# Kernel optimization log

Measured on AMD Instinct MI355X. Metric: run time of the kernel, lower is better.

The kernel has to match this reference:

```python
import jax, jax.numpy as jnp
import numpy as np

N = 50000        # nodes
E = 800000       # edges (before self-loops)
IN = 128         # in_dim
HID = 32         # hidden_dim per head
HEADS = 4
OUT = 64         # out_dim
NEG_SLOPE = 0.2  # PyG GATConv default leaky_relu slope


def setup_inputs() -> dict:
    key = jax.random.key(0)
    ks = jax.random.split(key, 10)
    g = lambda k, shape: jax.random.normal(k, shape, jnp.float32) * 0.1
    x = jax.random.normal(ks[0], (N, IN), jnp.float32)
    edge_index = jax.random.randint(ks[1], (2, E), 0, N, dtype=jnp.int64)
    W1 = g(ks[2], (IN, HEADS * HID))
    att_src1 = g(ks[3], (HEADS, HID))
    att_dst1 = g(ks[4], (HEADS, HID))
    b1 = jnp.zeros((HEADS * HID,), jnp.float32)
    W2 = g(ks[5], (HEADS * HID, OUT))
    att_src2 = g(ks[6], (1, OUT))
    att_dst2 = g(ks[7], (1, OUT))
    b2 = jnp.zeros((OUT,), jnp.float32)
    return {"x": x, "edge_index": edge_index,
            "W1": W1, "att_src1": att_src1, "att_dst1": att_dst1, "b1": b1,
            "W2": W2, "att_src2": att_src2, "att_dst2": att_dst2, "b2": b2}


def gat_layer(x, src, dst, W, a_src, a_dst, b, concat):
    """One PyG-style GATConv layer (self-loops already in src/dst)."""
    H, C = a_src.shape
    h = (x @ W).reshape(-1, H, C)                       # [N, H, C]
    al_s = jnp.sum(h * a_src, axis=-1)                  # [N, H]
    al_d = jnp.sum(h * a_dst, axis=-1)                  # [N, H]
    e = jax.nn.leaky_relu(al_s[src] + al_d[dst], NEG_SLOPE)  # [E', H]
    # segment softmax over incoming edges of each destination node
    m = jax.ops.segment_max(e, dst, num_segments=N)
    m = jnp.where(jnp.isfinite(m), m, 0.0)
    ex = jnp.exp(e - m[dst])
    denom = jax.ops.segment_sum(ex, dst, num_segments=N)
    alpha = ex / (denom[dst] + 1e-16)                   # [E', H]
    out = jax.ops.segment_sum(alpha[:, :, None] * h[src], dst, num_segments=N)  # [N,H,C]
    out = out.reshape(-1, H * C) if concat else out.mean(axis=1)
    return out + b


def reference(x, edge_index, W1, att_src1, att_dst1, b1, W2, att_src2, att_dst2, b2):
    src, dst = edge_index[0], edge_index[1]
    loop = jnp.arange(N, dtype=src.dtype)               # add_self_loops=True default
    src = jnp.concatenate([src, loop])
    dst = jnp.concatenate([dst, loop])
    h = gat_layer(x, src, dst, W1, att_src1, att_dst1, b1, concat=True)   # [N, HEADS*HID]
    h = jax.nn.elu(h)
    return gat_layer(h, src, dst, W2, att_src2, att_dst2, b2, concat=False)  # [N, OUT]
```

## Files before the change

kernel.cpp:

```cpp
#include <hip/hip_runtime.h>

#define NN 50000
#define EE 800000
#define NB 196
#define CHUNK 2048
#define NBLK ((EE + CHUNK - 1) / CHUNK)
#define GB1 ((NN + 63) / 64)
#define CAP 6144
#define CAPB 40
#define SSTR 6400

typedef unsigned int uint;
typedef unsigned short ushort;
typedef __attribute__((ext_vector_type(8))) short bf16x8;
typedef __attribute__((ext_vector_type(4))) float f32x4;

__device__ __forceinline__ float lrelu(float v){ return v > 0.f ? v : 0.2f*v; }
__device__ __forceinline__ ushort bf16r(float a){
  uint ua = __float_as_uint(a);
  return (ushort)((ua + 0x7FFFu + ((ua >> 16) & 1u)) >> 16);
}
__device__ __forceinline__ uint pack_bf16(float a, float b){
  return (uint)bf16r(a) | ((uint)bf16r(b) << 16);
}
__device__ __forceinline__ float bf_lo(uint u){ return __uint_as_float(u << 16); }
__device__ __forceinline__ float bf_hi(uint u){ return __uint_as_float(u & 0xFFFF0000u); }

union BG1Shared {
  struct { int h[NB]; int sc[256]; int gdelta[NB]; uint P[CHUNK]; int A[CHUNK]; } bk;
  struct { ushort Wt[128*136]; ushort Ash[64*136]; } gm;
};

__global__ __launch_bounds__(256, 3) void k_bg1(const int* __restrict__ ei,
    int* __restrict__ cnt, uint* __restrict__ ebuf,
    const float* __restrict__ x, const float* __restrict__ W,
    const float* __restrict__ a_src, const float* __restrict__ a_dst,
    uint* __restrict__ h1b, float* __restrict__ al_s, float* __restrict__ al_d,
    const float* __restrict__ W2, uint* __restrict__ w2b){
  __shared__ BG1Shared S;
  int t = threadIdx.x;
  if (blockIdx.x == NBLK + GB1){
    for (int idx = t; idx < 4096; idx += 256){
      int n = idx >> 6, kp = idx & 63;
      float a = W2[(2*kp)*64 + n];
      float b = W2[(2*kp+1)*64 + n];
      w2b[n*64 + kp] = pack_bf16(a, b);
    }
    return;
  }
  if (blockIdx.x < NBLK){
    if (t < NB) S.bk.h[t] = 0;
    __syncthreads();
    int base = blockIdx.x * CHUNK;
    int end = base + CHUNK; if (end > EE) end = EE;
    int bc = end - base;
    int be[8]; int re[8]; uint pe[8];
    #pragma unroll
    for (int q = 0; q < 8; ++q){
      int i = base + t + q*256;
      be[q] = -1;
      if (i < end){
        int s_ = ei[i], d_ = ei[EE + i];
        pe[q] = ((uint)d_ << 16) | (uint)s_;
        int bb = d_ >> 8;
        be[q] = bb;
        re[q] = atomicAdd(&S.bk.h[bb], 1);
      }
    }
    __syncthreads();
    int v = (t < NB) ? S.bk.h[t] : 0;
    S.bk.sc[t] = v;
    __syncthreads();
    for (int off = 1; off < 256; off <<= 1){
      int add = (t >= off) ? S.bk.sc[t-off] : 0;
      __syncthreads();
      S.bk.sc[t] += add;
      __syncthreads();
    }
    if (t < NB){
      int lofs = S.bk.sc[t] - v;
      S.bk.gdelta[t] = (t*NBLK + blockIdx.x)*CAPB - lofs;
      S.bk.h[t] = lofs;
      cnt[blockIdx.x*NB + t] = v;
    }
    __syncthreads();
    #pragma unroll
    for (int q = 0; q < 8; ++q) if (be[q] >= 0){
      int j = S.bk.h[be[q]] + re[q];
      S.bk.P[j] = pe[q];
      S.bk.A[j] = S.bk.gdelta[be[q]] + j;
    }
    __syncthreads();
    for (int j = t; j < bc; j += 256) ebuf[S.bk.A[j]] = S.bk.P[j];
    return;
  }
  int row0 = (blockIdx.x - NBLK) * 64;
  const float4* W4 = (const float4*)W;
  #pragma unroll
  for (int f0 = 0; f0 < 4096; f0 += 256){
    int idx4 = f0 + t;
    int k = idx4 >> 5;
    int n0 = (idx4 & 31) * 4;
    float4 v = W4[idx4];
    S.gm.Wt[(n0  )*136 + k] = bf16r(v.x);
    S.gm.Wt[(n0+1)*136 + k] = bf16r(v.y);
    S.gm.Wt[(n0+2)*136 + k] = bf16r(v.z);
    S.gm.Wt[(n0+3)*136 + k] = bf16r(v.w);
  }
  const float4* x4 = (const float4*)x;
  #pragma unroll
  for (int f0 = 0; f0 < 2048; f0 += 256){
    int idx4 = f0 + t;
    int row = idx4 >> 5;
    int q = idx4 & 31;
    float4 v = make_float4(0.f,0.f,0.f,0.f);
    if (row0 + row < NN) v = x4[(size_t)(row0+row)*32 + q];
    *(uint2*)(S.gm.Ash + row*136 + q*4) = make_uint2(pack_bf16(v.x, v.y), pack_bf16(v.z, v.w));
  }
  __syncthreads();

  int w = t >> 6, lane = t & 63;
  int lm = lane & 15, lg = lane >> 4;
  const ushort* Ab = S.gm.Ash + (w*16 + lm)*136 + lg*8;
  const ushort* Bb = S.gm.Wt + lm*136 + lg*8;
  f32x4 acc[8];
  #pragma unroll
  for (int i = 0; i < 8; ++i) acc[i] = (f32x4){0.f,0.f,0.f,0.f};
  #pragma unroll
  for (int ks = 0; ks < 4; ++ks){
    bf16x8 af = *(const bf16x8*)(Ab + ks*32);
    #pragma unroll
    for (int ct = 0; ct < 8; ++ct){
      bf16x8 bfr = *(const bf16x8*)(Bb + ct*16*136 + ks*32);
      acc[ct] = __builtin_amdgcn_mfma_f32_16x16x32_bf16(af, bfr, acc[ct], 0, 0, 0);
    }
  }
  int nbase = row0 + w*16 + lg*4;
  float ps[4][4], pd[4][4];
  #pragma unroll
  for (int h = 0; h < 4; ++h)
    #pragma unroll
    for (int r = 0; r < 4; ++r){ ps[h][r] = 0.f; pd[h][r] = 0.f; }
  #pragma unroll
  for (int ct = 0; ct < 8; ++ct){
    int col = ct*16 + lm;
    float ac = a_src[col], dc = a_dst[col];
    #pragma unroll
    for (int r = 0; r < 4; ++r){
      float v = acc[ct][r];
      ps[ct>>1][r] += v*ac;
      pd[ct>>1][r] += v*dc;
      float vp = __shfl_xor(v, 1);
      if ((lm & 1) == 0 && nbase + r < NN)
        h1b[(size_t)(nbase+r)*64 + ct*8 + (lm>>1)] = pack_bf16(v, vp);
    }
  }
  #pragma unroll
  for (int h = 0; h < 4; ++h)
    #pragma unroll
    for (int r = 0; r < 4; ++r){
      float s = ps[h][r], d = pd[h][r];
      s += __shfl_xor(s,1); s += __shfl_xor(s,2); s += __shfl_xor(s,4); s += __shfl_xor(s,8);
      d += __shfl_xor(d,1); d += __shfl_xor(d,2); d += __shfl_xor(d,4); d += __shfl_xor(d,8);
      if (lm == 0 && nbase + r < NN){
        al_s[(nbase+r)*4 + h] = s;
        al_d[(nbase+r)*4 + h] = d;
      }
    }
}

__global__ __launch_bounds__(256) void k_csr(const int* __restrict__ cnt,
                                             const uint* __restrict__ ebuf,
                                             int* __restrict__ rptr, int* __restrict__ rend,
                                             ushort* __restrict__ csr){
  __shared__ uint  sbuf[CAP];
  __shared__ ushort rnk[CAP];
  __shared__ int h[256];
  __shared__ int sc[256];
  __shared__ int btot;
  int b = blockIdx.x, t = threadIdx.x;
  int nd0 = b * 256;
  int ncnt = NN - nd0; if (ncnt > 256) ncnt = 256;
  int c0 = (t < NBLK) ? cnt[t*NB + b] : 0;
  int c1 = (t + 256 < NBLK) ? cnt[(t+256)*NB + b] : 0;
  if (c0 > CAPB) c0 = CAPB;
  if (c1 > CAPB) c1 = CAPB;
  int mysum = c0 + c1;
  sc[t] = mysum;
  __syncthreads();
  for (int off = 1; off < 256; off <<= 1){
    int add = (t >= off) ? sc[t-off] : 0;
    __syncthreads();
    sc[t] += add;
    __syncthreads();
  }
  int base = sc[t] - mysum;
  if (t == 255) btot = sc[255];
  __syncthreads();
  int tot = btot; if (tot > CAP) tot = CAP;
  for (int j = 0; j < c0; ++j)
    if (base + j < CAP) sbuf[base + j] = ebuf[(size_t)(b*NBLK + t)*CAPB + j];
  for (int j = 0; j < c1; ++j)
    if (base + c0 + j < CAP) sbuf[base + c0 + j] = ebuf[(size_t)(b*NBLK + t + 256)*CAPB + j];
  h[t] = (t < ncnt) ? 1 : 0;
  __syncthreads();
  for (int j = t; j < tot; j += 256){
    int local = (sbuf[j] >> 16) & 255;
    rnk[j] = (ushort)atomicAdd(&h[local], 1);
  }
  __syncthreads();
  int v = h[t];
  sc[t] = v;
  __syncthreads();
  for (int off = 1; off < 256; off <<= 1){
    int add = (t >= off) ? sc[t-off] : 0;
    __syncthreads();
    sc[t] += add;
    __syncthreads();
  }
  h[t] = sc[t] - v;
  __syncthreads();
  int cb = b * SSTR;
  if (t < ncnt){
    int rs = cb + h[t];
    rptr[nd0 + t] = rs;
    rend[nd0 + t] = rs + v;
    csr[rs] = (ushort)(nd0 + t);
  }
  for (int j = t; j < tot; j += 256){
    uint p = sbuf[j];
    int local = (p >> 16) & 255;
    csr[cb + h[local] + (int)rnk[j]] = (ushort)(p & 0xFFFFu);
  }
}

__global__ __launch_bounds__(512, 2) void k_ag12(const int* __restrict__ rptr, const int* __restrict__ rend,
    const ushort* __restrict__ csr,
    const uint* __restrict__ h1b, const float* __restrict__ al1s, const float* __restrict__ al1d,
    const float* __restrict__ b1, const uint* __restrict__ w2b,
    const float* __restrict__ a2s, const float* __restrict__ a2d,
    uint* __restrict__ gb, float* __restrict__ al2s, float* __restrict__ al2d){
  __shared__ ushort Wt[64*136];
  __shared__ ushort Ash[64*136];
  __shared__ float ssum[64], dsum[64];
  int tid = threadIdx.x;
  int nd0 = blockIdx.x * 64;
  if (tid < 64){ ssum[tid] = 0.f; dsum[tid] = 0.f; }
  const uint4* Wg = (const uint4*)w2b;
  #pragma unroll
  for (int f0 = 0; f0 < 1024; f0 += 512){
    int f = f0 + tid;
    int row = f >> 4, q = f & 15;
    uint4 v = Wg[f];
    *(uint4*)(Wt + row*136 + q*8) = v;
  }
  int w = tid >> 6, lane = tid & 63;
  int half = lane >> 5;
  int li   = lane & 31;
  int h    = li >> 3;
  uint rowoff = (uint)(li*2);
  uint* AshU = (uint*)Ash;
  for (int i = 0; i < 8; ++i){
    int nloc = w*8 + i;
    int wid = nd0 + nloc;
    if (wid >= NN) break;
    float ad = al1d[(uint)(wid*4 + h)];
    int rs = rptr[wid];
    int deg = rend[wid] - rs;
    float a0 = 0.f, a1 = 0.f, a2 = 0.f, a3 = 0.f, den = 0.f;
    for (int b0 = 0; b0 < deg; b0 += 64){
      int nb = deg - b0; if (nb > 64) nb = 64;
      int sv = (lane < nb) ? (int)csr[(uint)(rs + b0 + lane)] : 0;
      int jj = 0;
      for (; jj + 8 <= nb; jj += 8){
        int j = jj + half;
        int s0 = __shfl(sv, j), s1 = __shfl(sv, j+2), s2 = __shfl(sv, j+4), s3 = __shfl(sv, j+6);
        float e0 = al1s[(uint)(s0*4 + h)];
        float e1 = al1s[(uint)(s1*4 + h)];
        float e2 = al1s[(uint)(s2*4 + h)];
        float e3 = al1s[(uint)(s3*4 + h)];
        uint2 u0 = *(const uint2*)(h1b + (((uint)s0) << 6) + rowoff);
        uint2 u1 = *(const uint2*)(h1b + (((uint)s1) << 6) + rowoff);
        uint2 u2 = *(const uint2*)(h1b + (((uint)s2) << 6) + rowoff);
        uint2 u3 = *(const uint2*)(h1b + (((uint)s3) << 6) + rowoff);
        float x0 = __expf(lrelu(e0 + ad));
        float x1 = __expf(lrelu(e1 + ad));
        float x2 = __expf(lrelu(e2 + ad));
        float x3 = __expf(lrelu(e3 + ad));
        den += x0 + x1 + x2 + x3;
        a0 += x0*bf_lo(u0.x) + x1*bf_lo(u1.x) + x2*bf_lo(u2.x) + x3*bf_lo(u3.x);
        a1 += x0*bf_hi(u0.x) + x1*bf_hi(u1.x) + x2*bf_hi(u2.x) + x3*bf_hi(u3.x);
        a2 += x0*bf_lo(u0.y) + x1*bf_lo(u1.y) + x2*bf_lo(u2.y) + x3*bf_lo(u3.y);
        a3 += x0*bf_hi(u0.y) + x1*bf_hi(u1.y) + x2*bf_hi(u2.y) + x3*bf_hi(u3.y);
      }
      for (; jj < nb; jj += 2){
        int j = jj + half;
        bool ok = j < nb;
        int s0 = __shfl(sv, ok ? j : 0);
        float e = al1s[(uint)(s0*4 + h)];
        uint2 u = *(const uint2*)(h1b + (((uint)s0) << 6) + rowoff);
        float ex = ok ? __expf(lrelu(e + ad)) : 0.f;
        den += ex;
        a0 += ex*bf_lo(u.x); a1 += ex*bf_hi(u.x);
        a2 += ex*bf_lo(u.y); a3 += ex*bf_hi(u.y);
      }
    }
    den += __shfl_xor(den, 32);
    a0  += __shfl_xor(a0, 32);
    a1  += __shfl_xor(a1, 32);
    a2  += __shfl_xor(a2, 32);
    a3  += __shfl_xor(a3, 32);
    if (half == 0){
      float inv = 1.f/(den + 1e-16f);
      float4 bb = *(const float4*)(b1 + li*4);
      float o0 = a0*inv + bb.x, o1 = a1*inv + bb.y, o2 = a2*inv + bb.z, o3 = a3*inv + bb.w;
      o0 = o0 > 0.f ? o0 : (__expf(o0) - 1.f);
      o1 = o1 > 0.f ? o1 : (__expf(o1) - 1.f);
      o2 = o2 > 0.f ? o2 : (__expf(o2) - 1.f);
      o3 = o3 > 0.f ? o3 : (__expf(o3) - 1.f);
      *(uint2*)(AshU + nloc*68 + li*2) = make_uint2(pack_bf16(o0,o1), pack_bf16(o2,o3));
    }
  }
  __syncthreads();
  int lm = lane & 15, lg = lane >> 4;
  int rw = w & 3, cw = w >> 2;
  const ushort* Ab = Ash + (rw*16 + lm)*136 + lg*8;
  const ushort* Bb = Wt + (cw*32 + lm)*136 + lg*8;
  f32x4 acc[2];
  acc[0] = (f32x4){0.f,0.f,0.f,0.f};
  acc[1] = (f32x4){0.f,0.f,0.f,0.f};
  #pragma unroll
  for (int ks = 0; ks < 4; ++ks){
    bf16x8 af = *(const bf16x8*)(Ab + ks*32);
    #pragma unroll
    for (int ct = 0; ct < 2; ++ct){
      bf16x8 bfr = *(const bf16x8*)(Bb + ct*16*136 + ks*32);
      acc[ct] = __builtin_amdgcn_mfma_f32_16x16x32_bf16(af, bfr, acc[ct], 0, 0, 0);
    }
  }
  int nbase = nd0 + rw*16 + lg*4;
  float ps[4], pd[4];
  #pragma unroll
  for (int r = 0; r < 4; ++r){ ps[r] = 0.f; pd[r] = 0.f; }
  #pragma unroll
  for (int ct = 0; ct < 2; ++ct){
    int col = cw*32 + ct*16 + lm;
    float ac = a2s[col], dc = a2d[col];
    #pragma unroll
    for (int r = 0; r < 4; ++r){
      float v = acc[ct][r];
      ps[r] += v*ac;
      pd[r] += v*dc;
      float vp = __shfl_xor(v, 1);
      if ((lm & 1) == 0 && nbase + r < NN)
        gb[(size_t)(nbase+r)*32 + cw*16 + ct*8 + (lm>>1)] = pack_bf16(v, vp);
    }
  }
  #pragma unroll
  for (int r = 0; r < 4; ++r){
    float s = ps[r], d = pd[r];
    s += __shfl_xor(s,1); s += __shfl_xor(s,2); s += __shfl_xor(s,4); s += __shfl_xor(s,8);
    d += __shfl_xor(d,1); d += __shfl_xor(d,2); d += __shfl_xor(d,4); d += __shfl_xor(d,8);
    if (lm == 0){
      int nloc = rw*16 + lg*4 + r;
      atomicAdd(&ssum[nloc], s);
      atomicAdd(&dsum[nloc], d);
    }
  }
  __syncthreads();
  if (tid < 64 && nd0 + tid < NN){
    al2s[nd0 + tid] = ssum[tid];
    al2d[nd0 + tid] = dsum[tid];
  }
}

__global__ __launch_bounds__(256) void k_agg2(const int* __restrict__ rptr, const int* __restrict__ rend,
    const ushort* __restrict__ csr,
    const uint* __restrict__ gb, const float* __restrict__ al_s, const float* __restrict__ al_d,
    const float* __restrict__ b2, float* __restrict__ out){
  int wid  = (blockIdx.x*256 + threadIdx.x) >> 6;
  int lane = threadIdx.x & 63;
  if (wid >= NN) return;
  int half = lane >> 5;
  int li   = lane & 31;
  float ad = al_d[(uint)wid];
  int rs = rptr[wid];
  int deg = rend[wid] - rs;
  float a0 = 0.f, a1 = 0.f, den = 0.f;
  for (int b0 = 0; b0 < deg; b0 += 64){
    int nb = deg - b0; if (nb > 64) nb = 64;
    int sv = (lane < nb) ? (int)csr[(uint)(rs + b0 + lane)] : 0;
    int jj = 0;
    for (; jj + 8 <= nb; jj += 8){
      int j = jj + half;
      int s0 = __shfl(sv, j), s1 = __shfl(sv, j+2), s2 = __shfl(sv, j+4), s3 = __shfl(sv, j+6);
      float e0 = al_s[(uint)s0];
      float e1 = al_s[(uint)s1];
      float e2 = al_s[(uint)s2];
      float e3 = al_s[(uint)s3];
      uint u0 = gb[(((uint)s0) << 5) + (uint)li];
      uint u1 = gb[(((uint)s1) << 5) + (uint)li];
      uint u2 = gb[(((uint)s2) << 5) + (uint)li];
      uint u3 = gb[(((uint)s3) << 5) + (uint)li];
      float x0 = __expf(lrelu(e0 + ad));
      float x1 = __expf(lrelu(e1 + ad));
      float x2 = __expf(lrelu(e2 + ad));
      float x3 = __expf(lrelu(e3 + ad));
      den += x0 + x1 + x2 + x3;
      a0 += x0*bf_lo(u0) + x1*bf_lo(u1) + x2*bf_lo(u2) + x3*bf_lo(u3);
      a1 += x0*bf_hi(u0) + x1*bf_hi(u1) + x2*bf_hi(u2) + x3*bf_hi(u3);
    }
    for (; jj < nb; jj += 2){
      int j = jj + half;
      bool ok = j < nb;
      int s0 = __shfl(sv, ok ? j : 0);
      float e = al_s[(uint)s0];
      uint u = gb[(((uint)s0) << 5) + (uint)li];
      float ex = ok ? __expf(lrelu(e + ad)) : 0.f;
      den += ex;
      a0 += ex*bf_lo(u); a1 += ex*bf_hi(u);
    }
  }
  den += __shfl_xor(den, 32);
  a0  += __shfl_xor(a0, 32);
  a1  += __shfl_xor(a1, 32);
  if (half == 0){
    float inv = 1.f/(den + 1e-16f);
    float2 bb = *(const float2*)(b2 + li*2);
    *(float2*)(out + (size_t)wid*64 + li*2) = make_float2(a0*inv + bb.x, a1*inv + bb.y);
  }
}

extern "C" void kernel_launch(void* const* d_in, const int* in_sizes, int n_in,
                              void* d_out, int out_size, void* d_ws, size_t ws_size,
                              hipStream_t stream){
  const float* x   = (const float*)d_in[0];
  const int*   ei  = (const int*)d_in[1];
  const float* W1  = (const float*)d_in[2];
  const float* as1 = (const float*)d_in[3];
  const float* ad1 = (const float*)d_in[4];
  const float* b1  = (const float*)d_in[5];
  const float* W2  = (const float*)d_in[6];
  const float* as2 = (const float*)d_in[7];
  const float* ad2 = (const float*)d_in[8];
  const float* b2  = (const float*)d_in[9];
  float* out = (float*)d_out;
  (void)in_sizes; (void)n_in; (void)out_size; (void)ws_size;

  char* p = (char*)d_ws;
  size_t off = 0;
  auto alloc = [&](size_t bytes)->char*{
    char* r = p + off; off += (bytes + 255) & ~size_t(255); return r;
  };
  uint*  h1b   = (uint*)alloc((size_t)NN*64*4);
  uint*  gb    = (uint*)alloc((size_t)NN*32*4);
  uint*  w2b   = (uint*)alloc((size_t)64*64*4);
  float* al1s  = (float*)alloc((size_t)NN*4*4);
  float* al1d  = (float*)alloc((size_t)NN*4*4);
  float* al2s  = (float*)alloc((size_t)NN*4);
  float* al2d  = (float*)alloc((size_t)NN*4);
  int*   rptr  = (int*)alloc((size_t)NN*4);
  int*   rend  = (int*)alloc((size_t)NN*4);
  ushort* csr  = (ushort*)alloc((size_t)NB*SSTR*2);
  uint*  ebuf  = (uint*)alloc((size_t)NB*NBLK*CAPB*4);
  int*   cnt   = (int*)alloc((size_t)NBLK*NB*4);

  k_bg1<<<NBLK + GB1 + 1, 256, 0, stream>>>(ei, cnt, ebuf, x, W1, as1, ad1, h1b, al1s, al1d, W2, w2b);
  k_csr<<<NB, 256, 0, stream>>>(cnt, ebuf, rptr, rend, csr);
  k_ag12<<<GB1, 512, 0, stream>>>(rptr, rend, csr, h1b, al1s, al1d, b1, w2b, as2, ad2, gb, al2s, al2d);
  k_agg2<<<(NN*64+255)/256, 256, 0, stream>>>(rptr, rend, csr, gb, al2s, al2d, b2, out);
}
```

Baseline: 124.6 us.

## Load GEMM A-fragments directly from global and predicate aggregation tail loops

The layer-1 GEMM now reads each lane's x row slice straight from global memory into registers and converts it to bf16, instead of staging a 64-row x tile through shared memory. This shrinks the shared union enough to raise the occupancy hint from 3 to 4 blocks per CU. Both aggregation kernels replace the 8-wide main loop plus 2-wide remainder loop with one predicated 8-wide loop that masks out-of-range edges. The changes trade uncoalesced-ish direct global loads and some wasted masked gathers for less LDS traffic, fewer syncs and fewer tail iterations.

```diff
diff --git a/kernel.cpp b/kernel.cpp
--- a/kernel.cpp
+++ b/kernel.cpp
@@ -28,10 +28,10 @@
 
 union BG1Shared {
   struct { int h[NB]; int sc[256]; int gdelta[NB]; uint P[CHUNK]; int A[CHUNK]; } bk;
-  struct { ushort Wt[128*136]; ushort Ash[64*136]; } gm;
+  struct { ushort Wt[128*136]; } gm;
 };
 
-__global__ __launch_bounds__(256, 3) void k_bg1(const int* __restrict__ ei,
+__global__ __launch_bounds__(256, 4) void k_bg1(const int* __restrict__ ei,
     int* __restrict__ cnt, uint* __restrict__ ebuf,
     const float* __restrict__ x, const float* __restrict__ W,
     const float* __restrict__ a_src, const float* __restrict__ a_dst,
@@ -107,28 +107,25 @@
     S.gm.Wt[(n0+2)*136 + k] = bf16r(v.z);
     S.gm.Wt[(n0+3)*136 + k] = bf16r(v.w);
   }
-  const float4* x4 = (const float4*)x;
-  #pragma unroll
-  for (int f0 = 0; f0 < 2048; f0 += 256){
-    int idx4 = f0 + t;
-    int row = idx4 >> 5;
-    int q = idx4 & 31;
-    float4 v = make_float4(0.f,0.f,0.f,0.f);
-    if (row0 + row < NN) v = x4[(size_t)(row0+row)*32 + q];
-    *(uint2*)(S.gm.Ash + row*136 + q*4) = make_uint2(pack_bf16(v.x, v.y), pack_bf16(v.z, v.w));
-  }
   __syncthreads();
 
   int w = t >> 6, lane = t & 63;
   int lm = lane & 15, lg = lane >> 4;
-  const ushort* Ab = S.gm.Ash + (w*16 + lm)*136 + lg*8;
+  int myrow = row0 + w*16 + lm;
+  bool rok = myrow < NN;
+  const float* xrow = x + (size_t)(rok ? myrow : 0)*128 + lg*8;
   const ushort* Bb = S.gm.Wt + lm*136 + lg*8;
   f32x4 acc[8];
   #pragma unroll
   for (int i = 0; i < 8; ++i) acc[i] = (f32x4){0.f,0.f,0.f,0.f};
   #pragma unroll
   for (int ks = 0; ks < 4; ++ks){
-    bf16x8 af = *(const bf16x8*)(Ab + ks*32);
+    float4 f0 = rok ? *(const float4*)(xrow + ks*32)     : make_float4(0.f,0.f,0.f,0.f);
+    float4 f1 = rok ? *(const float4*)(xrow + ks*32 + 4) : make_float4(0.f,0.f,0.f,0.f);
+    union { uint4 u; bf16x8 v; } cvt;
+    cvt.u = make_uint4(pack_bf16(f0.x,f0.y), pack_bf16(f0.z,f0.w),
+                       pack_bf16(f1.x,f1.y), pack_bf16(f1.z,f1.w));
+    bf16x8 af = cvt.v;
     #pragma unroll
     for (int ct = 0; ct < 8; ++ct){
       bf16x8 bfr = *(const bf16x8*)(Bb + ct*16*136 + ks*32);
@@ -271,10 +268,11 @@
     for (int b0 = 0; b0 < deg; b0 += 64){
       int nb = deg - b0; if (nb > 64) nb = 64;
       int sv = (lane < nb) ? (int)csr[(uint)(rs + b0 + lane)] : 0;
-      int jj = 0;
-      for (; jj + 8 <= nb; jj += 8){
-        int j = jj + half;
-        int s0 = __shfl(sv, j), s1 = __shfl(sv, j+2), s2 = __shfl(sv, j+4), s3 = __shfl(sv, j+6);
+      for (int jj = 0; jj < nb; jj += 8){
+        int j0 = jj + half, j1 = j0 + 2, j2 = j0 + 4, j3 = j0 + 6;
+        bool k0 = j0 < nb, k1 = j1 < nb, k2 = j2 < nb, k3 = j3 < nb;
+        int s0 = __shfl(sv, k0 ? j0 : 0), s1 = __shfl(sv, k1 ? j1 : 0);
+        int s2 = __shfl(sv, k2 ? j2 : 0), s3 = __shfl(sv, k3 ? j3 : 0);
         float e0 = al1s[(uint)(s0*4 + h)];
         float e1 = al1s[(uint)(s1*4 + h)];
         float e2 = al1s[(uint)(s2*4 + h)];
@@ -283,26 +281,15 @@
         uint2 u1 = *(const uint2*)(h1b + (((uint)s1) << 6) + rowoff);
         uint2 u2 = *(const uint2*)(h1b + (((uint)s2) << 6) + rowoff);
         uint2 u3 = *(const uint2*)(h1b + (((uint)s3) << 6) + rowoff);
-        float x0 = __expf(lrelu(e0 + ad));
-        float x1 = __expf(lrelu(e1 + ad));
-        float x2 = __expf(lrelu(e2 + ad));
-        float x3 = __expf(lrelu(e3 + ad));
+        float x0 = k0 ? __expf(lrelu(e0 + ad)) : 0.f;
+        float x1 = k1 ? __expf(lrelu(e1 + ad)) : 0.f;
+        float x2 = k2 ? __expf(lrelu(e2 + ad)) : 0.f;
+        float x3 = k3 ? __expf(lrelu(e3 + ad)) : 0.f;
         den += x0 + x1 + x2 + x3;
         a0 += x0*bf_lo(u0.x) + x1*bf_lo(u1.x) + x2*bf_lo(u2.x) + x3*bf_lo(u3.x);
         a1 += x0*bf_hi(u0.x) + x1*bf_hi(u1.x) + x2*bf_hi(u2.x) + x3*bf_hi(u3.x);
         a2 += x0*bf_lo(u0.y) + x1*bf_lo(u1.y) + x2*bf_lo(u2.y) + x3*bf_lo(u3.y);
         a3 += x0*bf_hi(u0.y) + x1*bf_hi(u1.y) + x2*bf_hi(u2.y) + x3*bf_hi(u3.y);
-      }
-      for (; jj < nb; jj += 2){
-        int j = jj + half;
-        bool ok = j < nb;
-        int s0 = __shfl(sv, ok ? j : 0);
-        float e = al1s[(uint)(s0*4 + h)];
-        uint2 u = *(const uint2*)(h1b + (((uint)s0) << 6) + rowoff);
-        float ex = ok ? __expf(lrelu(e + ad)) : 0.f;
-        den += ex;
-        a0 += ex*bf_lo(u.x); a1 += ex*bf_hi(u.x);
-        a2 += ex*bf_lo(u.y); a3 += ex*bf_hi(u.y);
       }
     }
     den += __shfl_xor(den, 32);
@@ -390,10 +377,11 @@
   for (int b0 = 0; b0 < deg; b0 += 64){
     int nb = deg - b0; if (nb > 64) nb = 64;
     int sv = (lane < nb) ? (int)csr[(uint)(rs + b0 + lane)] : 0;
-    int jj = 0;
-    for (; jj + 8 <= nb; jj += 8){
-      int j = jj + half;
-      int s0 = __shfl(sv, j), s1 = __shfl(sv, j+2), s2 = __shfl(sv, j+4), s3 = __shfl(sv, j+6);
+    for (int jj = 0; jj < nb; jj += 8){
+      int j0 = jj + half, j1 = j0 + 2, j2 = j0 + 4, j3 = j0 + 6;
+      bool k0 = j0 < nb, k1 = j1 < nb, k2 = j2 < nb, k3 = j3 < nb;
+      int s0 = __shfl(sv, k0 ? j0 : 0), s1 = __shfl(sv, k1 ? j1 : 0);
+      int s2 = __shfl(sv, k2 ? j2 : 0), s3 = __shfl(sv, k3 ? j3 : 0);
       float e0 = al_s[(uint)s0];
       float e1 = al_s[(uint)s1];
       float e2 = al_s[(uint)s2];
@@ -402,23 +390,13 @@
       uint u1 = gb[(((uint)s1) << 5) + (uint)li];
       uint u2 = gb[(((uint)s2) << 5) + (uint)li];
       uint u3 = gb[(((uint)s3) << 5) + (uint)li];
-      float x0 = __expf(lrelu(e0 + ad));
-      float x1 = __expf(lrelu(e1 + ad));
-      float x2 = __expf(lrelu(e2 + ad));
-      float x3 = __expf(lrelu(e3 + ad));
+      float x0 = k0 ? __expf(lrelu(e0 + ad)) : 0.f;
+      float x1 = k1 ? __expf(lrelu(e1 + ad)) : 0.f;
+      float x2 = k2 ? __expf(lrelu(e2 + ad)) : 0.f;
+      float x3 = k3 ? __expf(lrelu(e3 + ad)) : 0.f;
       den += x0 + x1 + x2 + x3;
       a0 += x0*bf_lo(u0) + x1*bf_lo(u1) + x2*bf_lo(u2) + x3*bf_lo(u3);
       a1 += x0*bf_hi(u0) + x1*bf_hi(u1) + x2*bf_hi(u2) + x3*bf_hi(u3);
-    }
-    for (; jj < nb; jj += 2){
-      int j = jj + half;
-      bool ok = j < nb;
-      int s0 = __shfl(sv, ok ? j : 0);
-      float e = al_s[(uint)s0];
-      uint u = gb[(((uint)s0) << 5) + (uint)li];
-      float ex = ok ? __expf(lrelu(e + ad)) : 0.f;
-      den += ex;
-      a0 += ex*bf_lo(u); a1 += ex*bf_hi(u);
     }
   }
   den += __shfl_xor(den, 32);
```

After: 127.7 us. 2.5% more time.
